# Performance work log

Measured on AMD Instinct MI355X. Metric: run time of the kernel, lower is better.

The kernel has to match this reference:

```python
import jax, jax.numpy as jnp
import numpy as np

N = 100000      # nodes
E = 800000      # edges
D_IN = 128
H = 4           # heads
C = 32          # out channels per head (out_feature = H*C = 128)
EPS = 1e-5


def setup_inputs() -> dict:
    key = jax.random.key(0)
    ks = jax.random.split(key, 12)
    x = jax.random.normal(ks[0], (N, D_IN), dtype=jnp.float32)
    edge_index = jax.random.randint(ks[1], (2, E), 0, N, dtype=jnp.int32)
    edge_weights = jax.random.uniform(ks[2], (E, 1), dtype=jnp.float32)
    s = 1.0 / np.sqrt(D_IN)
    W_l = jax.random.uniform(ks[3], (D_IN, H * C), jnp.float32, -s, s)   # GATv2 lin_l (source)
    W_r = jax.random.uniform(ks[4], (D_IN, H * C), jnp.float32, -s, s)   # GATv2 lin_r (target)
    W_e = jax.random.uniform(ks[5], (1, H * C), jnp.float32, -1.0, 1.0)  # lin_edge (edge_dim=1)
    att = jax.random.uniform(ks[6], (H, C), jnp.float32, -s, s)          # attention vector
    bias = jnp.zeros((H * C,), jnp.float32)
    gamma = jnp.ones((H * C,), jnp.float32)   # BatchNorm weight
    beta = jnp.zeros((H * C,), jnp.float32)   # BatchNorm bias
    return {"x": x, "edge_index": edge_index, "edge_weights": edge_weights,
            "W_l": W_l, "W_r": W_r, "W_e": W_e, "att": att, "bias": bias,
            "gamma": gamma, "beta": beta}


def reference(x, edge_index, edge_weights, W_l, W_r, W_e, att, bias, gamma, beta):
    src = edge_index[0]  # message source j
    dst = edge_index[1]  # message target i (aggregation index)

    x_l = (x @ W_l).reshape(N, H, C)
    x_r = (x @ W_r).reshape(N, H, C)
    e = (edge_weights @ W_e).reshape(E, H, C)

    # GATv2 message: LeakyReLU(x_j + x_i + e, 0.2), score = <att, .>
    xj = x_l[src]                                  # [E,H,C]
    m = jax.nn.leaky_relu(xj + x_r[dst] + e, 0.2)  # [E,H,C]
    logits = jnp.einsum('ehc,hc->eh', m, att)      # [E,H]

    # segment softmax over edges sharing the same destination
    seg_max = jax.ops.segment_max(logits, dst, num_segments=N)  # [N,H]
    seg_max = jnp.where(jnp.isfinite(seg_max), seg_max, 0.0)
    expv = jnp.exp(logits - seg_max[dst])
    seg_sum = jax.ops.segment_sum(expv, dst, num_segments=N)
    alpha = expv / (seg_sum[dst] + 1e-16)          # [E,H]

    out = jax.ops.segment_sum(xj * alpha[:, :, None], dst, num_segments=N)  # [N,H,C]
    out = out.reshape(N, H * C) + bias

    # BatchNorm1d over nodes (training-mode batch statistics, biased var)
    mu = jnp.mean(out, axis=0)
    var = jnp.var(out, axis=0)
    out = gamma * (out - mu) * jax.lax.rsqrt(var + EPS) + beta

    # F.leaky_relu default negative_slope=0.01; dropout is identity in eval
    return jax.nn.leaky_relu(out, 0.01)
```

## Files before the change

kernel.cpp:

```cpp
#include <hip/hip_runtime.h>

#define D 128
#define HEADS 4

typedef __bf16 v8bf __attribute__((ext_vector_type(8)));
typedef float v4f __attribute__((ext_vector_type(4)));

__device__ __forceinline__ unsigned short f2bfbits(float f) {
    unsigned u = __float_as_uint(f);
    u += 0x7FFFu + ((u >> 16) & 1u);
    return (unsigned short)(u >> 16);
}

__device__ __forceinline__ float4 ldbf4(const __bf16* p) {
    const uint2 u = *reinterpret_cast<const uint2*>(p);
    float4 r;
    r.x = __uint_as_float(u.x << 16);
    r.y = __uint_as_float(u.x & 0xFFFF0000u);
    r.z = __uint_as_float(u.y << 16);
    r.w = __uint_as_float(u.y & 0xFFFF0000u);
    return r;
}

__global__ __launch_bounds__(256) void deg_wprep_k(
    const int* __restrict__ dst, int* __restrict__ deg, int E,
    const float* __restrict__ Wl, const float* __restrict__ Wr,
    __bf16* __restrict__ Wbf, int degBlocks) {
    if ((int)blockIdx.x < degBlocks) {
        const int e = blockIdx.x * 256 + threadIdx.x;
        if (e < E) atomicAdd(&deg[dst[e]], 1);
        return;
    }
    const int i = ((int)blockIdx.x - degBlocks) * 256 + threadIdx.x;
    const int cg = i >> 7;
    const int k = i & 127;
    const float* __restrict__ Wp = (cg < D) ? Wl : Wr;
    Wbf[i] = (__bf16)Wp[(size_t)k * D + (cg & (D - 1))];
}

__global__ __launch_bounds__(256) void scan1_k(
    const int* __restrict__ deg, int* __restrict__ rowptr,
    int* __restrict__ bsum, int n) {
    __shared__ int tmp[256];
    const int i = blockIdx.x * 256 + threadIdx.x;
    const int v = (i < n) ? deg[i] : 0;
    tmp[threadIdx.x] = v;
    __syncthreads();
    for (int off = 1; off < 256; off <<= 1) {
        int t = (threadIdx.x >= off) ? tmp[threadIdx.x - off] : 0;
        __syncthreads();
        tmp[threadIdx.x] += t;
        __syncthreads();
    }
    if (i < n) rowptr[i] = tmp[threadIdx.x] - v;
    if (threadIdx.x == 255) bsum[blockIdx.x] = tmp[255];
}

__global__ __launch_bounds__(256) void scan3_k(
    int* __restrict__ rowptr, const int* __restrict__ bsum,
    int* __restrict__ cursor, int n, int E) {
    __shared__ int wsum[4];
    int acc = 0;
    for (int j = threadIdx.x; j < blockIdx.x; j += 256) acc += bsum[j];
#pragma unroll
    for (int off = 1; off < 64; off <<= 1) acc += __shfl_xor(acc, off);
    if ((threadIdx.x & 63) == 0) wsum[threadIdx.x >> 6] = acc;
    __syncthreads();
    const int prefix = wsum[0] + wsum[1] + wsum[2] + wsum[3];
    const int i = blockIdx.x * 256 + threadIdx.x;
    if (i < n) {
        const int r = rowptr[i] + prefix;
        rowptr[i] = r;
        cursor[i] = r;
    } else if (i == n) {
        rowptr[n] = E;
    }
}

__global__ __launch_bounds__(256, 1) void gemm_fill_k(
    const float* __restrict__ x, const __bf16* __restrict__ Wbf,
    __bf16* __restrict__ xl, __bf16* __restrict__ xr, int n,
    const int* __restrict__ src, const int* __restrict__ dst,
    const float* __restrict__ ew, int* __restrict__ cursor,
    int2* __restrict__ epay, int E, int gemmBlocks) {
    if ((int)blockIdx.x >= gemmBlocks) {
        const int f = (int)blockIdx.x - gemmBlocks;
        const int xcd = f & 7;
        const int nchunk = ((int)gridDim.x - gemmBlocks) >> 3;
        const int slice = (n + 7) >> 3;
        const int lo = xcd * slice;
        const int hi = min(n, lo + slice);
        const int stride = nchunk * 256;
        for (int e = (f >> 3) * 256 + threadIdx.x; e < E; e += stride) {
            const int d = dst[e];
            if (d >= lo && d < hi) {
                const int p = atomicAdd(&cursor[d], 1);
                int2 v;
                v.x = src[e];
                v.y = __float_as_int(ew[e]);
                epay[p] = v;
            }
        }
        return;
    }
    __shared__ __align__(16) unsigned short cs[64 * 256];
    char* const xsb = (char*)cs;
    const int tid = threadIdx.x;
    const int row0 = blockIdx.x * 64;
    const int lane = tid & 63;
    const int wid = tid >> 6;
    const int col16 = lane & 15;
    const int kg = lane >> 4;

    for (int i = tid; i < 1024; i += 256) {
        const int r = i >> 4;
        const int k16 = (i & 15) * 16;
        const int row = row0 + r;
        float4 v0 = make_float4(0.f, 0.f, 0.f, 0.f), v1 = v0;
        if (row < n) {
            v0 = *reinterpret_cast<const float4*>(&x[(size_t)row * D + (i & 15) * 8]);
            v1 = *reinterpret_cast<const float4*>(&x[(size_t)row * D + (i & 15) * 8 + 4]);
        }
        uint4 p;
        p.x = ((unsigned)f2bfbits(v0.y) << 16) | f2bfbits(v0.x);
        p.y = ((unsigned)f2bfbits(v0.w) << 16) | f2bfbits(v0.z);
        p.z = ((unsigned)f2bfbits(v1.y) << 16) | f2bfbits(v1.x);
        p.w = ((unsigned)f2bfbits(v1.w) << 16) | f2bfbits(v1.z);
        *reinterpret_cast<uint4*>(xsb + (r * 256 + (k16 ^ ((r & 7) << 4)))) = p;
    }

    v8bf bfr[4][4];
#pragma unroll
    for (int nt = 0; nt < 4; ++nt) {
        const int cg = (wid * 4 + nt) * 16 + col16;
#pragma unroll
        for (int ks = 0; ks < 4; ++ks)
            bfr[nt][ks] = *reinterpret_cast<const v8bf*>(
                &Wbf[(size_t)cg * 128 + ks * 32 + kg * 8]);
    }
    __syncthreads();

    v4f acc[4][4] = {};
#pragma unroll
    for (int mt = 0; mt < 4; ++mt) {
        const int row = mt * 16 + col16;
        v8bf afr[4];
#pragma unroll
        for (int ks = 0; ks < 4; ++ks)
            afr[ks] = *reinterpret_cast<const v8bf*>(
                xsb + (row * 256 + ((ks * 64 + kg * 16) ^ ((row & 7) << 4))));
#pragma unroll
        for (int nt = 0; nt < 4; ++nt)
#pragma unroll
            for (int ks = 0; ks < 4; ++ks)
                acc[mt][nt] = __builtin_amdgcn_mfma_f32_16x16x32_bf16(
                    afr[ks], bfr[nt][ks], acc[mt][nt], 0, 0, 0);
    }

    __syncthreads();
#pragma unroll
    for (int mt = 0; mt < 4; ++mt)
#pragma unroll
        for (int nt = 0; nt < 4; ++nt) {
            const int cg = (wid * 4 + nt) * 16 + col16;
#pragma unroll
            for (int r = 0; r < 4; ++r)
                cs[(mt * 16 + kg * 4 + r) * 256 + cg] = f2bfbits(acc[mt][nt][r]);
        }
    __syncthreads();
    for (int i = tid; i < 2048; i += 256) {
        const int row = i >> 5;
        const int chunk = i & 31;
        const int gr = row0 + row;
        if (gr >= n) continue;
        const uint4 v = *reinterpret_cast<const uint4*>(&cs[row * 256 + chunk * 8]);
        if (chunk < 16)
            *reinterpret_cast<uint4*>(&xl[(size_t)gr * D + chunk * 8]) = v;
        else
            *reinterpret_cast<uint4*>(&xr[(size_t)gr * D + (chunk - 16) * 8]) = v;
    }
}

__global__ __launch_bounds__(256) void node_aggr_k(
    const __bf16* __restrict__ xl, const __bf16* __restrict__ xr,
    const int2* __restrict__ epay, const int* __restrict__ rowptr,
    const float* __restrict__ We, const float* __restrict__ att,
    __bf16* __restrict__ outb, int n) {
    const int wgl = (int)((blockIdx.x * (size_t)blockDim.x + threadIdx.x) >> 6);
    const int lane = threadIdx.x & 63;
    const int half = lane >> 5;
    const int node = wgl * 2 + half;
    const int ch = (lane & 31) * 4;

    int beg = 0, end = 0;
    if (node < n) {
        beg = rowptr[node];
        end = rowptr[node + 1];
    }
    const int dg = end - beg;
    const int tmax = max(dg, __shfl_xor(dg, 32));

    float4 b = make_float4(0.f, 0.f, 0.f, 0.f);
    if (node < n) b = ldbf4(&xr[(size_t)node * D + ch]);
    const float4 we4 = *reinterpret_cast<const float4*>(&We[ch]);
    const float4 at4 = *reinterpret_cast<const float4*>(&att[ch]);

    float s = 0.f;
    float4 acc = make_float4(0.f, 0.f, 0.f, 0.f);
    for (int t = 0; t < tmax; t += 2) {
        float part[2];
        float4 av[2];
#pragma unroll
        for (int i = 0; i < 2; ++i) {
            const int p = beg + t + i;
            const int q = max(min(p, end - 1), 0);
            const int2 pw = epay[q];
            av[i] = ldbf4(&xl[(size_t)pw.x * D + ch]);
            const float wgt = __int_as_float(pw.y);
            float c0 = fmaf(wgt, we4.x, av[i].x + b.x);
            float c1 = fmaf(wgt, we4.y, av[i].y + b.y);
            float c2 = fmaf(wgt, we4.z, av[i].z + b.z);
            float c3 = fmaf(wgt, we4.w, av[i].w + b.w);
            c0 = fmaxf(c0, 0.2f * c0);
            c1 = fmaxf(c1, 0.2f * c1);
            c2 = fmaxf(c2, 0.2f * c2);
            c3 = fmaxf(c3, 0.2f * c3);
            part[i] = fmaf(c3, at4.w, fmaf(c2, at4.z, fmaf(c1, at4.y, c0 * at4.x)));
        }
#pragma unroll
        for (int off = 1; off < 8; off <<= 1) {
            part[0] += __shfl_xor(part[0], off);
            part[1] += __shfl_xor(part[1], off);
        }
        const float pv0 = (t + 0 < dg) ? __expf(fminf(part[0], 50.f)) : 0.f;
        const float pv1 = (t + 1 < dg) ? __expf(fminf(part[1], 50.f)) : 0.f;
        s += pv0 + pv1;
        acc.x += fmaf(pv1, av[1].x, pv0 * av[0].x);
        acc.y += fmaf(pv1, av[1].y, pv0 * av[0].y);
        acc.z += fmaf(pv1, av[1].z, pv0 * av[0].z);
        acc.w += fmaf(pv1, av[1].w, pv0 * av[0].w);
    }
    if (node < n) {
        const float inv = 1.f / (s + 1e-16f);
        uint2 pkt;
        pkt.x = ((unsigned)f2bfbits(acc.y * inv) << 16) | f2bfbits(acc.x * inv);
        pkt.y = ((unsigned)f2bfbits(acc.w * inv) << 16) | f2bfbits(acc.z * inv);
        *reinterpret_cast<uint2*>(&outb[(size_t)node * D + ch]) = pkt;
    }
}

__global__ __launch_bounds__(256) void bn_partial_k(
    const __bf16* __restrict__ outb, float* __restrict__ sums,
    float* __restrict__ sumsq, int n) {
    __shared__ float rs[8][128];
    __shared__ float rq[8][128];
    const int c4 = (threadIdx.x & 31) * 4;
    const int rstr = threadIdx.x >> 5;
    float4 s = make_float4(0.f, 0.f, 0.f, 0.f);
    float4 q = make_float4(0.f, 0.f, 0.f, 0.f);
    for (int r = blockIdx.x * 8 + rstr; r < n; r += gridDim.x * 8) {
        const float4 v = ldbf4(&outb[(size_t)r * D + c4]);
        s.x += v.x; s.y += v.y; s.z += v.z; s.w += v.w;
        q.x = fmaf(v.x, v.x, q.x);
        q.y = fmaf(v.y, v.y, q.y);
        q.z = fmaf(v.z, v.z, q.z);
        q.w = fmaf(v.w, v.w, q.w);
    }
    rs[rstr][c4 + 0] = s.x; rs[rstr][c4 + 1] = s.y;
    rs[rstr][c4 + 2] = s.z; rs[rstr][c4 + 3] = s.w;
    rq[rstr][c4 + 0] = q.x; rq[rstr][c4 + 1] = q.y;
    rq[rstr][c4 + 2] = q.z; rq[rstr][c4 + 3] = q.w;
    __syncthreads();
    const int t = threadIdx.x;
    if (t < 128) {
        float a = 0.f;
#pragma unroll
        for (int j = 0; j < 8; ++j) a += rs[j][t];
        atomicAdd(&sums[t], a);
    } else {
        const int c = t - 128;
        float a = 0.f;
#pragma unroll
        for (int j = 0; j < 8; ++j) a += rq[j][c];
        atomicAdd(&sumsq[c], a);
    }
}

__global__ __launch_bounds__(256) void bn_apply_k(
    const __bf16* __restrict__ outb, float* __restrict__ out,
    const float* __restrict__ bnsums, const float* __restrict__ gamma,
    const float* __restrict__ beta, int n, int total4) {
    const int i = blockIdx.x * blockDim.x + threadIdx.x;
    if (i >= total4) return;
    const int c4 = (i & 31) * 4;
    const float inv_n = 1.f / (float)n;
    const float4 sm = *reinterpret_cast<const float4*>(&bnsums[c4]);
    const float4 sq = *reinterpret_cast<const float4*>(&bnsums[D + c4]);
    const float4 g = *reinterpret_cast<const float4*>(&gamma[c4]);
    const float4 bt = *reinterpret_cast<const float4*>(&beta[c4]);
    float4 v = ldbf4(&outb[(size_t)i * 4]);
    float mu, var, scale, shift, r;
    mu = sm.x * inv_n; var = fmaxf(sq.x * inv_n - mu * mu, 0.f);
    scale = g.x * rsqrtf(var + 1e-5f); shift = bt.x - mu * scale;
    r = fmaf(v.x, scale, shift); v.x = fmaxf(r, 0.01f * r);
    mu = sm.y * inv_n; var = fmaxf(sq.y * inv_n - mu * mu, 0.f);
    scale = g.y * rsqrtf(var + 1e-5f); shift = bt.y - mu * scale;
    r = fmaf(v.y, scale, shift); v.y = fmaxf(r, 0.01f * r);
    mu = sm.z * inv_n; var = fmaxf(sq.z * inv_n - mu * mu, 0.f);
    scale = g.z * rsqrtf(var + 1e-5f); shift = bt.z - mu * scale;
    r = fmaf(v.z, scale, shift); v.z = fmaxf(r, 0.01f * r);
    mu = sm.w * inv_n; var = fmaxf(sq.w * inv_n - mu * mu, 0.f);
    scale = g.w * rsqrtf(var + 1e-5f); shift = bt.w - mu * scale;
    r = fmaf(v.w, scale, shift); v.w = fmaxf(r, 0.01f * r);
    *reinterpret_cast<float4*>(&out[(size_t)i * 4]) = v;
}

extern "C" void kernel_launch(void* const* d_in, const int* in_sizes, int n_in,
                              void* d_out, int out_size, void* d_ws, size_t ws_size,
                              hipStream_t stream) {
    const float* x     = (const float*)d_in[0];
    const int*   ei    = (const int*)d_in[1];
    const float* ew    = (const float*)d_in[2];
    const float* Wl    = (const float*)d_in[3];
    const float* Wr    = (const float*)d_in[4];
    const float* We    = (const float*)d_in[5];
    const float* att   = (const float*)d_in[6];
    const float* gamma = (const float*)d_in[8];
    const float* beta  = (const float*)d_in[9];

    const int n = in_sizes[0] / D;
    const int E = in_sizes[2];
    const int* src = ei;
    const int* dst = ei + E;
    const int nblk = (n + 255) / 256;

    char* ws = (char*)d_ws;
    size_t off = 0;
    __bf16* xl = (__bf16*)(ws + off);   off += (size_t)n * D * 2;
    __bf16* xr = (__bf16*)(ws + off);   off += (size_t)n * D * 2;
    __bf16* outb = (__bf16*)(ws + off); off += (size_t)n * D * 2;
    __bf16* Wbf = (__bf16*)(ws + off);  off += (size_t)2 * D * D * 2;
    float* bnsums = (float*)(ws + off); off += 2 * D * sizeof(float);
    int* deg = (int*)(ws + off);        off += (size_t)n * sizeof(int);
    int* rowptr = (int*)(ws + off);     off += ((size_t)n + 1) * sizeof(int);
    int* cursor = (int*)(ws + off);     off += (size_t)n * sizeof(int);
    int* bsum = (int*)(ws + off);       off += (size_t)nblk * sizeof(int);
    off = (off + 15) & ~(size_t)15;
    int2* epay = (int2*)(ws + off);     off += (size_t)E * sizeof(int2);

    float* outacc = (float*)d_out;

    hipMemsetAsync(bnsums, 0, (2 * D + (size_t)n) * sizeof(float), stream);

    const int degBlocks = (E + 255) / 256;
    deg_wprep_k<<<degBlocks + 128, 256, 0, stream>>>(dst, deg, E, Wl, Wr, Wbf,
                                                     degBlocks);

    scan1_k<<<nblk, 256, 0, stream>>>(deg, rowptr, bsum, n);
    scan3_k<<<nblk + 1, 256, 0, stream>>>(rowptr, bsum, cursor, n, E);

    const int gemmBlocks = (n + 63) / 64;
    gemm_fill_k<<<gemmBlocks + 2048, 256, 0, stream>>>(
        x, Wbf, xl, xr, n, src, dst, ew, cursor, epay, E, gemmBlocks);

    const int waves = (n + 1) / 2;
    node_aggr_k<<<(waves + 3) / 4, 256, 0, stream>>>(xl, xr, epay, rowptr,
                                                     We, att, outb, n);

    bn_partial_k<<<512, 256, 0, stream>>>(outb, bnsums, bnsums + D, n);
    bn_apply_k<<<((n * D / 4) + 255) / 256, 256, 0, stream>>>(
        outb, outacc, bnsums, gamma, beta, n, n * D / 4);
}
```

Before: 194.6 us.

## Shrink GEMM shared tile with padding and store outputs directly from registers

Replaces the 32KB XOR-swizzled shared buffer with a 17KB padded [64][136] tile for the A operand. The epilogue no longer stages results in shared memory for coalesced 16-byte stores; each lane writes scalar bf16 values straight to xl/xr. This drops two barriers and the minimum-occupancy launch bound, so more blocks can fit per CU. The cost is strided 2-byte global stores, which may coalesce poorly.

```diff
diff --git a/kernel.cpp b/kernel.cpp
--- a/kernel.cpp
+++ b/kernel.cpp
@@ -77,7 +77,7 @@
     }
 }
 
-__global__ __launch_bounds__(256, 1) void gemm_fill_k(
+__global__ __launch_bounds__(256) void gemm_fill_k(
     const float* __restrict__ x, const __bf16* __restrict__ Wbf,
     __bf16* __restrict__ xl, __bf16* __restrict__ xr, int n,
     const int* __restrict__ src, const int* __restrict__ dst,
@@ -103,8 +103,7 @@
         }
         return;
     }
-    __shared__ __align__(16) unsigned short cs[64 * 256];
-    char* const xsb = (char*)cs;
+    __shared__ __align__(16) unsigned short xs[64][136];
     const int tid = threadIdx.x;
     const int row0 = blockIdx.x * 64;
     const int lane = tid & 63;
@@ -114,19 +113,19 @@
 
     for (int i = tid; i < 1024; i += 256) {
         const int r = i >> 4;
-        const int k16 = (i & 15) * 16;
+        const int k0 = (i & 15) * 8;
         const int row = row0 + r;
         float4 v0 = make_float4(0.f, 0.f, 0.f, 0.f), v1 = v0;
         if (row < n) {
-            v0 = *reinterpret_cast<const float4*>(&x[(size_t)row * D + (i & 15) * 8]);
-            v1 = *reinterpret_cast<const float4*>(&x[(size_t)row * D + (i & 15) * 8 + 4]);
+            v0 = *reinterpret_cast<const float4*>(&x[(size_t)row * D + k0]);
+            v1 = *reinterpret_cast<const float4*>(&x[(size_t)row * D + k0 + 4]);
         }
         uint4 p;
         p.x = ((unsigned)f2bfbits(v0.y) << 16) | f2bfbits(v0.x);
         p.y = ((unsigned)f2bfbits(v0.w) << 16) | f2bfbits(v0.z);
         p.z = ((unsigned)f2bfbits(v1.y) << 16) | f2bfbits(v1.x);
         p.w = ((unsigned)f2bfbits(v1.w) << 16) | f2bfbits(v1.z);
-        *reinterpret_cast<uint4*>(xsb + (r * 256 + (k16 ^ ((r & 7) << 4)))) = p;
+        *reinterpret_cast<uint4*>(&xs[r][k0]) = p;
     }
 
     v8bf bfr[4][4];
@@ -143,12 +142,10 @@
     v4f acc[4][4] = {};
 #pragma unroll
     for (int mt = 0; mt < 4; ++mt) {
-        const int row = mt * 16 + col16;
         v8bf afr[4];
 #pragma unroll
         for (int ks = 0; ks < 4; ++ks)
-            afr[ks] = *reinterpret_cast<const v8bf*>(
-                xsb + (row * 256 + ((ks * 64 + kg * 16) ^ ((row & 7) << 4))));
+            afr[ks] = *reinterpret_cast<const v8bf*>(&xs[mt * 16 + col16][ks * 32 + kg * 8]);
 #pragma unroll
         for (int nt = 0; nt < 4; ++nt)
 #pragma unroll
@@ -157,28 +154,19 @@
                     afr[ks], bfr[nt][ks], acc[mt][nt], 0, 0, 0);
     }
 
-    __syncthreads();
 #pragma unroll
     for (int mt = 0; mt < 4; ++mt)
 #pragma unroll
         for (int nt = 0; nt < 4; ++nt) {
             const int cg = (wid * 4 + nt) * 16 + col16;
-#pragma unroll
-            for (int r = 0; r < 4; ++r)
-                cs[(mt * 16 + kg * 4 + r) * 256 + cg] = f2bfbits(acc[mt][nt][r]);
-        }
-    __syncthreads();
-    for (int i = tid; i < 2048; i += 256) {
-        const int row = i >> 5;
-        const int chunk = i & 31;
-        const int gr = row0 + row;
-        if (gr >= n) continue;
-        const uint4 v = *reinterpret_cast<const uint4*>(&cs[row * 256 + chunk * 8]);
-        if (chunk < 16)
-            *reinterpret_cast<uint4*>(&xl[(size_t)gr * D + chunk * 8]) = v;
-        else
-            *reinterpret_cast<uint4*>(&xr[(size_t)gr * D + (chunk - 16) * 8]) = v;
-    }
+            __bf16* __restrict__ op = (cg < D) ? xl : xr;
+            const int c = cg & (D - 1);
+#pragma unroll
+            for (int r = 0; r < 4; ++r) {
+                const int row = row0 + mt * 16 + kg * 4 + r;
+                if (row < n) op[(size_t)row * D + c] = (__bf16)acc[mt][nt][r];
+            }
+        }
 }
 
 __global__ __launch_bounds__(256) void node_aggr_k(
```

New measurement: 196.5 us. Within noise of the previous version (+1.0%).
